# Optimization experiments

Hardware: AMD Instinct MI355X
Metric: run time of the kernel (lower is better)

The kernel has to match this reference:

```python
import jax, jax.numpy as jnp
import numpy as np

B, L, D_ENC = 32, 512, 512
STEPS = 32
E_DIM = 128      # embedding_dim
A_DIM = 256      # attention_dim
H = 512          # hidden_size
VOCAB = 32000


def _linear(x, W, b):
    return x @ W.T + b


def setup_inputs() -> dict:
    key = jax.random.key(0)
    ks = jax.random.split(key, 12)
    s = lambda fan_in: 1.0 / np.sqrt(fan_in)
    return {
        "encoder_outputs": jax.random.normal(ks[0], (B, L, D_ENC), dtype=jnp.float32),
        "target_seq": jax.random.randint(ks[1], (B, STEPS), 0, VOCAB, dtype=jnp.int64),
        "pos_embedding": jax.random.normal(ks[2], (STEPS, E_DIM), dtype=jnp.float32),
        "dec_proj_W": jax.random.uniform(ks[3], (A_DIM, E_DIM), minval=-s(E_DIM), maxval=s(E_DIM)),
        "dec_proj_b": jnp.zeros((A_DIM,), jnp.float32),
        "enc_proj_W": jax.random.uniform(ks[4], (A_DIM, D_ENC), minval=-s(D_ENC), maxval=s(D_ENC)),
        "enc_proj_b": jnp.zeros((A_DIM,), jnp.float32),
        "attn_score_W": jax.random.uniform(ks[5], (1, A_DIM), minval=-s(A_DIM), maxval=s(A_DIM)),
        "attn_score_b": jnp.zeros((1,), jnp.float32),
        "hidden_proj_W": jax.random.uniform(ks[6], (H, E_DIM), minval=-s(E_DIM), maxval=s(E_DIM)),
        "hidden_proj_b": jnp.zeros((H,), jnp.float32),
        "fc_out_W": jax.random.uniform(ks[7], (VOCAB, H + D_ENC), minval=-s(H + D_ENC), maxval=s(H + D_ENC)),
        "fc_out_b": jnp.zeros((VOCAB,), jnp.float32),
    }


def reference(encoder_outputs, target_seq, pos_embedding,
              dec_proj_W, dec_proj_b, enc_proj_W, enc_proj_b,
              attn_score_W, attn_score_b, hidden_proj_W, hidden_proj_b,
              fc_out_W, fc_out_b):
    batch = encoder_outputs.shape[0]
    steps = target_seq.shape[1]
    # [B, L, A]
    enc_proj = _linear(encoder_outputs, enc_proj_W, enc_proj_b)
    # [B, S, E]  (dropout=0 in eval)
    pos_emb = jnp.broadcast_to(pos_embedding[:steps][None], (batch, steps, pos_embedding.shape[1]))
    # [B, S, A]
    dec_query = _linear(pos_emb, dec_proj_W, dec_proj_b)
    # additive attention: [B, S, L, A]
    combined = jnp.tanh(enc_proj[:, None, :, :] + dec_query[:, :, None, :])
    # score reduction to scalar: [B, S, L]
    attn_scores = jnp.einsum('bsla,a->bsl', combined, attn_score_W[0]) + attn_score_b[0]
    attn_weights = jax.nn.softmax(attn_scores, axis=2)
    # context: [B, S, D_enc]
    context = jnp.einsum('bsl,bld->bsd', attn_weights, encoder_outputs)
    hidden = _linear(pos_emb, hidden_proj_W, hidden_proj_b)  # [B, S, H]
    logits = _linear(jnp.concatenate([hidden, context], axis=-1), fc_out_W, fc_out_b)
    return logits
```

## Files before the change

### kernel.cpp

```cpp
#include <hip/hip_runtime.h>
#include <hip/hip_bf16.h>
#include <stdint.h>

typedef __attribute__((ext_vector_type(4))) float f32x4;
typedef __attribute__((ext_vector_type(8))) short short8;

#define B_   32
#define L_   512
#define DE_  512
#define S_   32
#define ED_  128
#define AD_  256
#define HD_  512
#define VOC_ 32000
#define M_   1024

__device__ __forceinline__ unsigned short f2bf(float f){
  union { float f; unsigned int u; } v; v.f = f;
  unsigned int u = v.u;
  unsigned int r = (u + 0x7FFFu + ((u >> 16) & 1u)) >> 16;
  return (unsigned short)r;
}

__device__ __forceinline__ float bf2f(unsigned short u){
  union { unsigned int u; float f; } v; v.u = ((unsigned int)u) << 16;
  return v.f;
}

__device__ __forceinline__ float tanh_fast(float x){
  float t = __expf(2.0f * x);
  return (t - 1.0f) * __builtin_amdgcn_rcpf(t + 1.0f);
}

__device__ __forceinline__ void gl_lds16(const void* g, void* l){
  __builtin_amdgcn_global_load_lds(
      (const __attribute__((address_space(1))) unsigned int*)g,
      (__attribute__((address_space(3))) unsigned int*)l, 16, 0, 0);
}

extern "C" __global__ void __launch_bounds__(256)
k_cvt(const float* __restrict__ src, unsigned short* __restrict__ dst, int n4){
  int stride = gridDim.x * 256;
  for (int i = blockIdx.x * 256 + threadIdx.x; i < n4; i += stride){
    f32x4 v = ((const f32x4*)src)[i];
    ushort4 o;
    o.x = f2bf(v[0]); o.y = f2bf(v[1]); o.z = f2bf(v[2]); o.w = f2bf(v[3]);
    ((ushort4*)dst)[i] = o;
  }
}

extern "C" __global__ void __launch_bounds__(256)
k_small(const float* __restrict__ pos, const float* __restrict__ dW, const float* __restrict__ db,
        const float* __restrict__ hW, const float* __restrict__ hb,
        float* __restrict__ dq, unsigned short* __restrict__ hbf){
  int t = blockIdx.x * 256 + threadIdx.x;
  if (t < S_ * AD_){
    int s = t >> 8, a = t & 255;
    const float* p = pos + s * ED_;
    const float* wrow = dW + a * ED_;
    float acc = db[a];
    #pragma unroll 4
    for (int e = 0; e < ED_; ++e) acc += p[e] * wrow[e];
    dq[t] = acc;
  } else if (t < S_ * AD_ + S_ * HD_){
    int u = t - S_ * AD_;
    int s = u >> 9, h = u & 511;
    const float* p = pos + s * ED_;
    const float* wrow = hW + h * ED_;
    float acc = hb[h];
    #pragma unroll 4
    for (int e = 0; e < ED_; ++e) acc += p[e] * wrow[e];
    hbf[u] = f2bf(acc);
  }
}

extern "C" __global__ void __launch_bounds__(256)
k_gemm_encp(const unsigned short* __restrict__ A, const unsigned short* __restrict__ Bt,
            const float* __restrict__ bias, unsigned short* __restrict__ C){
  __shared__ unsigned short As[128 * 32];
  __shared__ unsigned short Bs[128 * 32];
  int bm = blockIdx.x >> 1, bn = blockIdx.x & 1;
  int tid = threadIdx.x, wid = tid >> 6, lane = tid & 63;
  int fr = lane & 15, fq = lane >> 4;
  int wm = wid >> 1, wn = wid & 1;
  f32x4 acc[4][4];
  #pragma unroll
  for (int i = 0; i < 4; ++i)
    #pragma unroll
    for (int j = 0; j < 4; ++j) acc[i][j] = (f32x4)0.0f;

  for (int k0 = 0; k0 < 512; k0 += 32){
    __syncthreads();
    #pragma unroll
    for (int i = 0; i < 2; ++i){
      int seg = wid * 2 + i;
      int row = seg * 16 + (lane >> 2);
      int col = (lane & 3) * 8;
      gl_lds16(A  + (size_t)(bm * 128 + row) * 512 + k0 + col, &As[seg * 512]);
      gl_lds16(Bt + (size_t)(bn * 128 + row) * 512 + k0 + col, &Bs[seg * 512]);
    }
    __syncthreads();
    short8 a[4], b[4];
    #pragma unroll
    for (int mf = 0; mf < 4; ++mf) a[mf] = *(const short8*)&As[(wm * 64 + mf * 16 + fr) * 32 + fq * 8];
    #pragma unroll
    for (int nf = 0; nf < 4; ++nf) b[nf] = *(const short8*)&Bs[(wn * 64 + nf * 16 + fr) * 32 + fq * 8];
    #pragma unroll
    for (int mf = 0; mf < 4; ++mf)
      #pragma unroll
      for (int nf = 0; nf < 4; ++nf)
        acc[mf][nf] = __builtin_amdgcn_mfma_f32_16x16x32_bf16(a[mf], b[nf], acc[mf][nf], 0, 0, 0);
  }
  #pragma unroll
  for (int mf = 0; mf < 4; ++mf){
    int row = bm * 128 + wm * 64 + mf * 16 + fq * 4;
    #pragma unroll
    for (int nf = 0; nf < 4; ++nf){
      int col = bn * 128 + wn * 64 + nf * 16 + fr;
      float bv = bias[col];
      #pragma unroll
      for (int j = 0; j < 4; ++j)
        C[(size_t)(row + j) * 256 + col] = f2bf(acc[mf][nf][j] + bv);
    }
  }
}

extern "C" __global__ void __launch_bounds__(256)
k_attn(const unsigned short* __restrict__ encp, const float* __restrict__ dq,
       const float* __restrict__ vW, float* __restrict__ wgt){
  int idx = blockIdx.x;
  int wg = (idx & 7) * 128 + (idx >> 3);
  int b = wg >> 5, s = wg & 31;
  int tid = threadIdx.x, wid = tid >> 6, lane = tid & 63;
  int half = lane >> 5, a0 = (lane & 31) * 8;
  __shared__ float sc[512];
  __shared__ float redm[4], reds[4];
  f32x4 dqa = *(const f32x4*)&dq[s * AD_ + a0];
  f32x4 dqb = *(const f32x4*)&dq[s * AD_ + a0 + 4];
  f32x4 va  = *(const f32x4*)&vW[a0];
  f32x4 vb  = *(const f32x4*)&vW[a0 + 4];
  for (int it = 0; it < 64; ++it){
    int l = wid * 128 + it * 2 + half;
    short8 e8 = *(const short8*)&encp[((size_t)(b * 512 + l)) * 256 + a0];
    float p = 0.0f;
    #pragma unroll
    for (int j = 0; j < 4; ++j) p += tanh_fast(bf2f((unsigned short)e8[j]) + dqa[j]) * va[j];
    #pragma unroll
    for (int j = 0; j < 4; ++j) p += tanh_fast(bf2f((unsigned short)e8[4 + j]) + dqb[j]) * vb[j];
    #pragma unroll
    for (int off = 16; off >= 1; off >>= 1) p += __shfl_xor(p, off);
    if ((lane & 31) == 0) sc[l] = p;
  }
  __syncthreads();
  float s0 = sc[tid], s1 = sc[tid + 256];
  float m = fmaxf(s0, s1);
  #pragma unroll
  for (int off = 32; off >= 1; off >>= 1) m = fmaxf(m, __shfl_xor(m, off));
  if (lane == 0) redm[wid] = m;
  __syncthreads();
  m = fmaxf(fmaxf(redm[0], redm[1]), fmaxf(redm[2], redm[3]));
  float e0 = __expf(s0 - m), e1 = __expf(s1 - m);
  float sum = e0 + e1;
  #pragma unroll
  for (int off = 32; off >= 1; off >>= 1) sum += __shfl_xor(sum, off);
  if (lane == 0) reds[wid] = sum;
  __syncthreads();
  float tot = reds[0] + reds[1] + reds[2] + reds[3];
  float inv = __builtin_amdgcn_rcpf(tot);
  size_t base = (size_t)(b * 32 + s) * 512;
  wgt[base + tid] = e0 * inv;
  wgt[base + tid + 256] = e1 * inv;
}

extern "C" __global__ void __launch_bounds__(256)
k_ctx(const unsigned short* __restrict__ encb, const float* __restrict__ wgt,
      unsigned short* __restrict__ ctx){
  int b = blockIdx.x >> 4, dt = blockIdx.x & 15;
  int tid = threadIdx.x;
  __shared__ float wl[32 * 512];
  #pragma unroll 8
  for (int i = 0; i < 64; ++i)
    wl[i * 256 + tid] = wgt[(size_t)b * 16384 + i * 256 + tid];
  __syncthreads();
  int d = dt * 32 + (tid & 31);
  int grp = tid >> 5;
  float acc0 = 0, acc1 = 0, acc2 = 0, acc3 = 0;
  const unsigned short* ebase = encb + (size_t)b * 262144 + d;
  const float* w0 = &wl[(grp * 4 + 0) * 512];
  const float* w1 = &wl[(grp * 4 + 1) * 512];
  const float* w2 = &wl[(grp * 4 + 2) * 512];
  const float* w3 = &wl[(grp * 4 + 3) * 512];
  #pragma unroll 8
  for (int l = 0; l < 512; ++l){
    float e = bf2f(ebase[(size_t)l * 512]);
    acc0 += w0[l] * e; acc1 += w1[l] * e; acc2 += w2[l] * e; acc3 += w3[l] * e;
  }
  size_t obase = (size_t)(b * 32 + grp * 4) * 512 + d;
  ctx[obase]        = f2bf(acc0);
  ctx[obase + 512]  = f2bf(acc1);
  ctx[obase + 1024] = f2bf(acc2);
  ctx[obase + 1536] = f2bf(acc3);
}

extern "C" __global__ void __launch_bounds__(256)
k_wprep(const float* __restrict__ fcW, const unsigned short* __restrict__ hbf,
        const float* __restrict__ fcb, unsigned short* __restrict__ Wc,
        float* __restrict__ logh){
  int bn = blockIdx.x;
  int tid = threadIdx.x, wid = tid >> 6, lane = tid & 63;
  int fr = lane & 15, fq = lane >> 4;
  #pragma unroll 8
  for (int i = 0; i < 32; ++i){
    int idx = i * 256 + tid;
    int row = idx >> 7, c4 = idx & 127;
    f32x4 v = *(const f32x4*)&fcW[(size_t)(bn * 64 + row) * 1024 + 512 + c4 * 4];
    ushort4 o;
    o.x = f2bf(v[0]); o.y = f2bf(v[1]); o.z = f2bf(v[2]); o.w = f2bf(v[3]);
    *(ushort4*)&Wc[(size_t)(bn * 64 + row) * 512 + c4 * 4] = o;
  }
  int col = bn * 64 + wid * 16 + fr;
  const float* brow = fcW + (size_t)col * 1024;
  f32x4 acc0 = (f32x4)0.0f, acc1 = (f32x4)0.0f;
  #pragma unroll 4
  for (int k0 = 0; k0 < 512; k0 += 32){
    int ko = k0 + fq * 8;
    f32x4 b0 = *(const f32x4*)(brow + ko);
    f32x4 b1 = *(const f32x4*)(brow + ko + 4);
    short8 bfr;
    bfr[0] = (short)f2bf(b0[0]); bfr[1] = (short)f2bf(b0[1]);
    bfr[2] = (short)f2bf(b0[2]); bfr[3] = (short)f2bf(b0[3]);
    bfr[4] = (short)f2bf(b1[0]); bfr[5] = (short)f2bf(b1[1]);
    bfr[6] = (short)f2bf(b1[2]); bfr[7] = (short)f2bf(b1[3]);
    short8 a0 = *(const short8*)&hbf[(size_t)fr * 512 + ko];
    short8 a1 = *(const short8*)&hbf[(size_t)(16 + fr) * 512 + ko];
    acc0 = __builtin_amdgcn_mfma_f32_16x16x32_bf16(a0, bfr, acc0, 0, 0, 0);
    acc1 = __builtin_amdgcn_mfma_f32_16x16x32_bf16(a1, bfr, acc1, 0, 0, 0);
  }
  float bv = fcb[col];
  #pragma unroll
  for (int j = 0; j < 4; ++j){
    logh[(size_t)(fq * 4 + j) * VOC_ + col]      = acc0[j] + bv;
    logh[(size_t)(16 + fq * 4 + j) * VOC_ + col] = acc1[j] + bv;
  }
}

extern "C" __global__ void __launch_bounds__(512, 2)
k_gemm_main(const unsigned short* __restrict__ Abf, const unsigned short* __restrict__ Wc,
            const float* __restrict__ logh, float* __restrict__ out){
  __shared__ unsigned short As[2][256 * 32];
  __shared__ unsigned short Bs[3][256 * 32];
  int orig = blockIdx.x;
  int xcd = orig & 7, j = orig >> 3;
  int wgid = (xcd < 4 ? xcd * 63 : 252 + (xcd - 4) * 62) + j;
  int bm = wgid & 3, bn = wgid >> 2;
  int tid = threadIdx.x, wid = tid >> 6, lane = tid & 63;
  int fr = lane & 15, fq = lane >> 4;
  int wm = wid >> 2, wn = wid & 3;
  int abase = bm * 256, bbase = bn * 256;
  int srow = lane >> 2;
  int scol = ((lane & 3) ^ ((lane >> 3) & 3)) * 8;
  int c0 = wid * 2;
  const unsigned short* aS0 = Abf + (size_t)(abase + c0 * 16 + srow) * 512 + scol;
  const unsigned short* aS1 = aS0 + (size_t)16 * 512;
  const unsigned short* bS0 = Wc  + (size_t)(bbase + c0 * 16 + srow) * 512 + scol;
  const unsigned short* bS1 = bS0 + (size_t)16 * 512;
  int swzfq = (fq ^ ((fr >> 1) & 3)) * 8;

  f32x4 acc[8][4];
  #pragma unroll
  for (int i = 0; i < 8; ++i)
    #pragma unroll
    for (int jj = 0; jj < 4; ++jj) acc[i][jj] = (f32x4)0.0f;

#define STAGE_A(buf, kk) do { \
    gl_lds16(aS0 + (kk), &As[buf][c0 * 512]); \
    gl_lds16(aS1 + (kk), &As[buf][c0 * 512 + 512]); \
  } while (0)
#define STAGE_B(buf, kk) do { \
    gl_lds16(bS0 + (kk), &Bs[buf][c0 * 512]); \
    gl_lds16(bS1 + (kk), &Bs[buf][c0 * 512 + 512]); \
  } while (0)

  STAGE_A(0, 0);
  STAGE_B(0, 0);
  STAGE_B(1, 32);
  asm volatile("s_waitcnt vmcnt(2)" ::: "memory");
  __builtin_amdgcn_s_barrier();
  __builtin_amdgcn_sched_barrier(0);

  #pragma unroll
  for (int t = 0; t < 16; ++t){
    const int ca = t & 1, cb = t % 3;
    short8 a[8], b[4];
    if (t < 15) STAGE_A(ca ^ 1, (size_t)(t + 1) * 32);
    #pragma unroll
    for (int nf = 0; nf < 4; ++nf)
      b[nf] = *(const short8*)&Bs[cb][(wn * 64 + nf * 16 + fr) * 32 + swzfq];
    #pragma unroll
    for (int mf = 0; mf < 4; ++mf)
      a[mf] = *(const short8*)&As[ca][(wm * 128 + mf * 16 + fr) * 32 + swzfq];
    __builtin_amdgcn_s_setprio(1);
    #pragma unroll
    for (int mf = 0; mf < 4; ++mf)
      #pragma unroll
      for (int nf = 0; nf < 4; ++nf)
        acc[mf][nf] = __builtin_amdgcn_mfma_f32_16x16x32_bf16(a[mf], b[nf], acc[mf][nf], 0, 0, 0);
    __builtin_amdgcn_s_setprio(0);
    if (t < 14) STAGE_B((t + 2) % 3, (size_t)(t + 2) * 32);
    #pragma unroll
    for (int mf = 4; mf < 8; ++mf)
      a[mf] = *(const short8*)&As[ca][(wm * 128 + mf * 16 + fr) * 32 + swzfq];
    __builtin_amdgcn_s_setprio(1);
    #pragma unroll
    for (int mf = 4; mf < 8; ++mf)
      #pragma unroll
      for (int nf = 0; nf < 4; ++nf)
        acc[mf][nf] = __builtin_amdgcn_mfma_f32_16x16x32_bf16(a[mf], b[nf], acc[mf][nf], 0, 0, 0);
    __builtin_amdgcn_s_setprio(0);
    if (t < 14)      asm volatile("s_waitcnt vmcnt(2)" ::: "memory");
    else if (t == 14) asm volatile("s_waitcnt vmcnt(0)" ::: "memory");
    if (t < 15){
      __builtin_amdgcn_s_barrier();
      __builtin_amdgcn_sched_barrier(0);
    }
  }
#undef STAGE_A
#undef STAGE_B

  #pragma unroll
  for (int mf = 0; mf < 8; ++mf){
    int rowb = bm * 256 + wm * 128 + mf * 16 + fq * 4;
    #pragma unroll
    for (int nf = 0; nf < 4; ++nf){
      int col = bn * 256 + wn * 64 + nf * 16 + fr;
      #pragma unroll
      for (int jj = 0; jj < 4; ++jj){
        int r = rowb + jj;
        out[(size_t)r * VOC_ + col] = acc[mf][nf][jj] + logh[(size_t)(r & 31) * VOC_ + col];
      }
    }
  }
}

extern "C" void kernel_launch(void* const* d_in, const int* in_sizes, int n_in,
                              void* d_out, int out_size, void* d_ws, size_t ws_size,
                              hipStream_t stream){
  const float* enc = (const float*)d_in[0];
  const float* pos = (const float*)d_in[2];
  const float* dW  = (const float*)d_in[3];
  const float* db  = (const float*)d_in[4];
  const float* eW  = (const float*)d_in[5];
  const float* eb  = (const float*)d_in[6];
  const float* vW  = (const float*)d_in[7];
  const float* hW  = (const float*)d_in[9];
  const float* hb  = (const float*)d_in[10];
  const float* fcW = (const float*)d_in[11];
  const float* fcb = (const float*)d_in[12];
  float* out = (float*)d_out;

  char* w = (char*)d_ws;
  unsigned short* Wc_bf   = (unsigned short*)(w);
  unsigned short* enc_bf  = (unsigned short*)(w + 32768000);
  unsigned short* encp_bf = (unsigned short*)(w + 49545216);
  unsigned short* ctx     = (unsigned short*)(w + 57933824);
  float*          logh    = (float*)(w + 58982400);
  float*          dq      = (float*)(w + 63078400);
  unsigned short* hbf     = (unsigned short*)(w + 63111168);
  unsigned short* encW_bf = (unsigned short*)(w + 63143936);
  float*          wgt     = (float*)(w + 63406080);

  k_cvt<<<dim3(2048), dim3(256), 0, stream>>>(enc, enc_bf, 8388608 / 4);
  k_cvt<<<dim3(128), dim3(256), 0, stream>>>(eW, encW_bf, 131072 / 4);
  k_small<<<dim3(96), dim3(256), 0, stream>>>(pos, dW, db, hW, hb, dq, hbf);
  k_gemm_encp<<<dim3(256), dim3(256), 0, stream>>>(enc_bf, encW_bf, eb, encp_bf);
  k_attn<<<dim3(1024), dim3(256), 0, stream>>>(encp_bf, dq, vW, wgt);
  k_ctx<<<dim3(512), dim3(256), 0, stream>>>(enc_bf, wgt, ctx);
  k_wprep<<<dim3(500), dim3(256), 0, stream>>>(fcW, hbf, fcb, Wc_bf, logh);
  k_gemm_main<<<dim3(500), dim3(512), 0, stream>>>(ctx, Wc_bf, logh, out);
}
```

Baseline: 210.6 us.

## Fuse prep kernels, double-buffer encoder GEMM, halve main GEMM M-tile

Merges the two conversion kernels and the small projection kernel into one launch to cut launch overhead. It also gives the encoder-projection GEMM double-buffered, swizzled LDS staging with one barrier per k-step. The main logits GEMM moves from 256x256 to 128x256 tiles over 1000 blocks with a simpler XCD block mapping, aiming for better occupancy and load balance. The smaller tile lowers per-block reuse of the fc weight and doubles how often the weight tiles are loaded.

```diff
diff --git a/kernel.cpp b/kernel.cpp
--- a/kernel.cpp
+++ b/kernel.cpp
@@ -39,78 +39,100 @@
 }
 
 extern "C" __global__ void __launch_bounds__(256)
-k_cvt(const float* __restrict__ src, unsigned short* __restrict__ dst, int n4){
-  int stride = gridDim.x * 256;
-  for (int i = blockIdx.x * 256 + threadIdx.x; i < n4; i += stride){
-    f32x4 v = ((const f32x4*)src)[i];
+k_prep(const float* __restrict__ enc, unsigned short* __restrict__ enc_bf,
+       const float* __restrict__ eW, unsigned short* __restrict__ encW_bf,
+       const float* __restrict__ pos,
+       const float* __restrict__ dW, const float* __restrict__ db,
+       const float* __restrict__ hW, const float* __restrict__ hb,
+       float* __restrict__ dq, unsigned short* __restrict__ hbf){
+  int blk = blockIdx.x, tid = threadIdx.x;
+  if (blk < 8192){
+    int i = blk * 256 + tid;
+    f32x4 v = ((const f32x4*)enc)[i];
     ushort4 o;
     o.x = f2bf(v[0]); o.y = f2bf(v[1]); o.z = f2bf(v[2]); o.w = f2bf(v[3]);
-    ((ushort4*)dst)[i] = o;
-  }
-}
-
-extern "C" __global__ void __launch_bounds__(256)
-k_small(const float* __restrict__ pos, const float* __restrict__ dW, const float* __restrict__ db,
-        const float* __restrict__ hW, const float* __restrict__ hb,
-        float* __restrict__ dq, unsigned short* __restrict__ hbf){
-  int t = blockIdx.x * 256 + threadIdx.x;
-  if (t < S_ * AD_){
-    int s = t >> 8, a = t & 255;
-    const float* p = pos + s * ED_;
-    const float* wrow = dW + a * ED_;
-    float acc = db[a];
-    #pragma unroll 4
-    for (int e = 0; e < ED_; ++e) acc += p[e] * wrow[e];
-    dq[t] = acc;
-  } else if (t < S_ * AD_ + S_ * HD_){
-    int u = t - S_ * AD_;
-    int s = u >> 9, h = u & 511;
-    const float* p = pos + s * ED_;
-    const float* wrow = hW + h * ED_;
-    float acc = hb[h];
-    #pragma unroll 4
-    for (int e = 0; e < ED_; ++e) acc += p[e] * wrow[e];
-    hbf[u] = f2bf(acc);
-  }
-}
-
-extern "C" __global__ void __launch_bounds__(256)
+    ((ushort4*)enc_bf)[i] = o;
+  } else if (blk < 8320){
+    int i = (blk - 8192) * 256 + tid;
+    f32x4 v = ((const f32x4*)eW)[i];
+    ushort4 o;
+    o.x = f2bf(v[0]); o.y = f2bf(v[1]); o.z = f2bf(v[2]); o.w = f2bf(v[3]);
+    ((ushort4*)encW_bf)[i] = o;
+  } else {
+    int t = (blk - 8320) * 256 + tid;
+    if (t < S_ * AD_){
+      int s = t >> 8, a = t & 255;
+      const float* p = pos + s * ED_;
+      const float* wrow = dW + a * ED_;
+      float acc = db[a];
+      #pragma unroll 4
+      for (int e = 0; e < ED_; ++e) acc += p[e] * wrow[e];
+      dq[t] = acc;
+    } else if (t < S_ * AD_ + S_ * HD_){
+      int u = t - S_ * AD_;
+      int s = u >> 9, h = u & 511;
+      const float* p = pos + s * ED_;
+      const float* wrow = hW + h * ED_;
+      float acc = hb[h];
+      #pragma unroll 4
+      for (int e = 0; e < ED_; ++e) acc += p[e] * wrow[e];
+      hbf[u] = f2bf(acc);
+    }
+  }
+}
+
+extern "C" __global__ void __launch_bounds__(256, 4)
 k_gemm_encp(const unsigned short* __restrict__ A, const unsigned short* __restrict__ Bt,
             const float* __restrict__ bias, unsigned short* __restrict__ C){
-  __shared__ unsigned short As[128 * 32];
-  __shared__ unsigned short Bs[128 * 32];
+  __shared__ unsigned short As[2][128 * 32];
+  __shared__ unsigned short Bs[2][128 * 32];
   int bm = blockIdx.x >> 1, bn = blockIdx.x & 1;
   int tid = threadIdx.x, wid = tid >> 6, lane = tid & 63;
   int fr = lane & 15, fq = lane >> 4;
   int wm = wid >> 1, wn = wid & 1;
+  int srow = lane >> 2;
+  int scol = ((lane & 3) ^ ((lane >> 3) & 3)) * 8;
+  int c0 = wid * 2;
+  const unsigned short* aS0 = A  + (size_t)(bm * 128 + c0 * 16 + srow) * 512 + scol;
+  const unsigned short* aS1 = aS0 + (size_t)16 * 512;
+  const unsigned short* bS0 = Bt + (size_t)(bn * 128 + c0 * 16 + srow) * 512 + scol;
+  const unsigned short* bS1 = bS0 + (size_t)16 * 512;
+  int swzfq = (fq ^ ((fr >> 1) & 3)) * 8;
+
   f32x4 acc[4][4];
   #pragma unroll
   for (int i = 0; i < 4; ++i)
     #pragma unroll
     for (int j = 0; j < 4; ++j) acc[i][j] = (f32x4)0.0f;
 
-  for (int k0 = 0; k0 < 512; k0 += 32){
-    __syncthreads();
-    #pragma unroll
-    for (int i = 0; i < 2; ++i){
-      int seg = wid * 2 + i;
-      int row = seg * 16 + (lane >> 2);
-      int col = (lane & 3) * 8;
-      gl_lds16(A  + (size_t)(bm * 128 + row) * 512 + k0 + col, &As[seg * 512]);
-      gl_lds16(Bt + (size_t)(bn * 128 + row) * 512 + k0 + col, &Bs[seg * 512]);
-    }
-    __syncthreads();
+#define STAGE_E(buf, kk) do { \
+    gl_lds16(aS0 + (kk), &As[buf][c0 * 512]); \
+    gl_lds16(aS1 + (kk), &As[buf][c0 * 512 + 512]); \
+    gl_lds16(bS0 + (kk), &Bs[buf][c0 * 512]); \
+    gl_lds16(bS1 + (kk), &Bs[buf][c0 * 512 + 512]); \
+  } while (0)
+
+  STAGE_E(0, 0);
+  __syncthreads();
+
+  int cur = 0;
+  for (int t = 0; t < 16; ++t){
+    if (t < 15) STAGE_E(cur ^ 1, (size_t)(t + 1) * 32);
     short8 a[4], b[4];
     #pragma unroll
-    for (int mf = 0; mf < 4; ++mf) a[mf] = *(const short8*)&As[(wm * 64 + mf * 16 + fr) * 32 + fq * 8];
-    #pragma unroll
-    for (int nf = 0; nf < 4; ++nf) b[nf] = *(const short8*)&Bs[(wn * 64 + nf * 16 + fr) * 32 + fq * 8];
+    for (int mf = 0; mf < 4; ++mf) a[mf] = *(const short8*)&As[cur][(wm * 64 + mf * 16 + fr) * 32 + swzfq];
+    #pragma unroll
+    for (int nf = 0; nf < 4; ++nf) b[nf] = *(const short8*)&Bs[cur][(wn * 64 + nf * 16 + fr) * 32 + swzfq];
     #pragma unroll
     for (int mf = 0; mf < 4; ++mf)
       #pragma unroll
       for (int nf = 0; nf < 4; ++nf)
         acc[mf][nf] = __builtin_amdgcn_mfma_f32_16x16x32_bf16(a[mf], b[nf], acc[mf][nf], 0, 0, 0);
-  }
+    __syncthreads();
+    cur ^= 1;
+  }
+#undef STAGE_E
+
   #pragma unroll
   for (int mf = 0; mf < 4; ++mf){
     int row = bm * 128 + wm * 64 + mf * 16 + fq * 4;
@@ -244,41 +266,35 @@
   }
 }
 
-extern "C" __global__ void __launch_bounds__(512, 2)
+extern "C" __global__ void __launch_bounds__(512, 4)
 k_gemm_main(const unsigned short* __restrict__ Abf, const unsigned short* __restrict__ Wc,
             const float* __restrict__ logh, float* __restrict__ out){
-  __shared__ unsigned short As[2][256 * 32];
+  __shared__ unsigned short As[2][128 * 32];
   __shared__ unsigned short Bs[3][256 * 32];
   int orig = blockIdx.x;
-  int xcd = orig & 7, j = orig >> 3;
-  int wgid = (xcd < 4 ? xcd * 63 : 252 + (xcd - 4) * 62) + j;
-  int bm = wgid & 3, bn = wgid >> 2;
+  int wg = (orig & 7) * 125 + (orig >> 3);
+  int bm = wg & 7, bn = wg >> 3;
   int tid = threadIdx.x, wid = tid >> 6, lane = tid & 63;
   int fr = lane & 15, fq = lane >> 4;
   int wm = wid >> 2, wn = wid & 3;
-  int abase = bm * 256, bbase = bn * 256;
+  int abase = bm * 128, bbase = bn * 256;
   int srow = lane >> 2;
   int scol = ((lane & 3) ^ ((lane >> 3) & 3)) * 8;
-  int c0 = wid * 2;
-  const unsigned short* aS0 = Abf + (size_t)(abase + c0 * 16 + srow) * 512 + scol;
-  const unsigned short* aS1 = aS0 + (size_t)16 * 512;
-  const unsigned short* bS0 = Wc  + (size_t)(bbase + c0 * 16 + srow) * 512 + scol;
+  const unsigned short* aS0 = Abf + (size_t)(abase + wid * 16 + srow) * 512 + scol;
+  const unsigned short* bS0 = Wc  + (size_t)(bbase + wid * 32 + srow) * 512 + scol;
   const unsigned short* bS1 = bS0 + (size_t)16 * 512;
   int swzfq = (fq ^ ((fr >> 1) & 3)) * 8;
 
-  f32x4 acc[8][4];
-  #pragma unroll
-  for (int i = 0; i < 8; ++i)
+  f32x4 acc[4][4];
+  #pragma unroll
+  for (int i = 0; i < 4; ++i)
     #pragma unroll
     for (int jj = 0; jj < 4; ++jj) acc[i][jj] = (f32x4)0.0f;
 
-#define STAGE_A(buf, kk) do { \
-    gl_lds16(aS0 + (kk), &As[buf][c0 * 512]); \
-    gl_lds16(aS1 + (kk), &As[buf][c0 * 512 + 512]); \
-  } while (0)
+#define STAGE_A(buf, kk) gl_lds16(aS0 + (kk), &As[buf][wid * 512])
 #define STAGE_B(buf, kk) do { \
-    gl_lds16(bS0 + (kk), &Bs[buf][c0 * 512]); \
-    gl_lds16(bS1 + (kk), &Bs[buf][c0 * 512 + 512]); \
+    gl_lds16(bS0 + (kk), &Bs[buf][wid * 1024]); \
+    gl_lds16(bS1 + (kk), &Bs[buf][wid * 1024 + 512]); \
   } while (0)
 
   STAGE_A(0, 0);
@@ -291,33 +307,33 @@
   #pragma unroll
   for (int t = 0; t < 16; ++t){
     const int ca = t & 1, cb = t % 3;
-    short8 a[8], b[4];
+    short8 a[4], b[4];
     if (t < 15) STAGE_A(ca ^ 1, (size_t)(t + 1) * 32);
     #pragma unroll
     for (int nf = 0; nf < 4; ++nf)
       b[nf] = *(const short8*)&Bs[cb][(wn * 64 + nf * 16 + fr) * 32 + swzfq];
     #pragma unroll
-    for (int mf = 0; mf < 4; ++mf)
-      a[mf] = *(const short8*)&As[ca][(wm * 128 + mf * 16 + fr) * 32 + swzfq];
+    for (int mf = 0; mf < 2; ++mf)
+      a[mf] = *(const short8*)&As[ca][(wm * 64 + mf * 16 + fr) * 32 + swzfq];
     __builtin_amdgcn_s_setprio(1);
     #pragma unroll
-    for (int mf = 0; mf < 4; ++mf)
+    for (int mf = 0; mf < 2; ++mf)
       #pragma unroll
       for (int nf = 0; nf < 4; ++nf)
         acc[mf][nf] = __builtin_amdgcn_mfma_f32_16x16x32_bf16(a[mf], b[nf], acc[mf][nf], 0, 0, 0);
     __builtin_amdgcn_s_setprio(0);
     if (t < 14) STAGE_B((t + 2) % 3, (size_t)(t + 2) * 32);
     #pragma unroll
-    for (int mf = 4; mf < 8; ++mf)
-      a[mf] = *(const short8*)&As[ca][(wm * 128 + mf * 16 + fr) * 32 + swzfq];
+    for (int mf = 2; mf < 4; ++mf)
+      a[mf] = *(const short8*)&As[ca][(wm * 64 + mf * 16 + fr) * 32 + swzfq];
     __builtin_amdgcn_s_setprio(1);
     #pragma unroll
-    for (int mf = 4; mf < 8; ++mf)
+    for (int mf = 2; mf < 4; ++mf)
       #pragma unroll
       for (int nf = 0; nf < 4; ++nf)
         acc[mf][nf] = __builtin_amdgcn_mfma_f32_16x16x32_bf16(a[mf], b[nf], acc[mf][nf], 0, 0, 0);
     __builtin_amdgcn_s_setprio(0);
-    if (t < 14)      asm volatile("s_waitcnt vmcnt(2)" ::: "memory");
+    if (t < 14)       asm volatile("s_waitcnt vmcnt(2)" ::: "memory");
     else if (t == 14) asm volatile("s_waitcnt vmcnt(0)" ::: "memory");
     if (t < 15){
       __builtin_amdgcn_s_barrier();
@@ -328,8 +344,8 @@
 #undef STAGE_B
 
   #pragma unroll
-  for (int mf = 0; mf < 8; ++mf){
-    int rowb = bm * 256 + wm * 128 + mf * 16 + fq * 4;
+  for (int mf = 0; mf < 4; ++mf){
+    int rowb = bm * 128 + wm * 64 + mf * 16 + fq * 4;
     #pragma unroll
     for (int nf = 0; nf < 4; ++nf){
       int col = bn * 256 + wn * 64 + nf * 16 + fr;
@@ -369,12 +385,11 @@
   unsigned short* encW_bf = (unsigned short*)(w + 63143936);
   float*          wgt     = (float*)(w + 63406080);
 
-  k_cvt<<<dim3(2048), dim3(256), 0, stream>>>(enc, enc_bf, 8388608 / 4);
-  k_cvt<<<dim3(128), dim3(256), 0, stream>>>(eW, encW_bf, 131072 / 4);
-  k_small<<<dim3(96), dim3(256), 0, stream>>>(pos, dW, db, hW, hb, dq, hbf);
+  k_prep<<<dim3(8416), dim3(256), 0, stream>>>(enc, enc_bf, eW, encW_bf,
+                                               pos, dW, db, hW, hb, dq, hbf);
   k_gemm_encp<<<dim3(256), dim3(256), 0, stream>>>(enc_bf, encW_bf, eb, encp_bf);
   k_attn<<<dim3(1024), dim3(256), 0, stream>>>(encp_bf, dq, vW, wgt);
   k_ctx<<<dim3(512), dim3(256), 0, stream>>>(enc_bf, wgt, ctx);
   k_wprep<<<dim3(500), dim3(256), 0, stream>>>(fcW, hbf, fcb, Wc_bf, logh);
-  k_gemm_main<<<dim3(500), dim3(512), 0, stream>>>(ctx, Wc_bf, logh, out);
-}
+  k_gemm_main<<<dim3(1000), dim3(512), 0, stream>>>(ctx, Wc_bf, logh, out);
+}
```

New measurement: 209.3 us. About the same (-0.6%).
